# Kernel optimization log

Hardware: AMD Instinct MI355X
Metric: run time of the kernel (lower is better)

Reference implementation:

```python
import jax, jax.numpy as jnp
import numpy as np

EPS = 1e-20


def _conv(x, w, pad):
    # NCHW / OIHW conv, stride 1, symmetric padding
    return jax.lax.conv_general_dilated(
        x, w, window_strides=(1, 1),
        padding=((pad, pad), (pad, pad)),
        dimension_numbers=("NCHW", "OIHW", "NCHW"))


def _nconv(data, conf, w, b, pad):
    # normalized convolution: conv(d*c)/conv(c) + bias ; cout = conv(c)/sum(w)
    denom = _conv(conf, w, pad)
    nomin = _conv(data * conf, w, pad)
    out = nomin / (denom + EPS) + b[None, :, None, None]
    s = jnp.sum(w, axis=(1, 2, 3))  # per-out-channel kernel sum
    cout = denom / s[None, :, None, None]
    return out, cout


def _maxpool_ds(x, c):
    # 2x2/stride-2 max pool on c, gathering x at argmax positions (torch return_indices semantics)
    B, C, H, W = c.shape
    cw = c.reshape(B, C, H // 2, 2, W // 2, 2).transpose(0, 1, 2, 4, 3, 5).reshape(B, C, H // 2, W // 2, 4)
    xw = x.reshape(B, C, H // 2, 2, W // 2, 2).transpose(0, 1, 2, 4, 3, 5).reshape(B, C, H // 2, W // 2, 4)
    idx = jnp.argmax(cw, axis=-1)  # first-max tie-break, same as torch
    c_ds = jnp.take_along_axis(cw, idx[..., None], axis=-1)[..., 0] / 4.0
    x_ds = jnp.take_along_axis(xw, idx[..., None], axis=-1)[..., 0]
    return x_ds, c_ds


def _up2(x):
    return jnp.repeat(jnp.repeat(x, 2, axis=2), 2, axis=3)


def setup_inputs() -> dict:
    key = jax.random.key(0)
    ks = jax.random.split(key, 18)
    B, H, W = 8, 512, 512
    x0 = jax.random.normal(ks[0], (B, 1, H, W), dtype=jnp.float32)
    c0 = jax.random.uniform(ks[1], (B, 1, H, W), dtype=jnp.float32)

    def posw(k, shape):
        # positive kernel (the module enforces positivity via softplus hook)
        return jax.nn.softplus(jax.random.normal(k, shape, dtype=jnp.float32))

    inp = {"x0": x0, "c0": c0}
    shapes = {
        "w1": (2, 1, 5, 5), "w2": (2, 2, 5, 5), "w3": (2, 2, 5, 5),
        "w4": (2, 4, 3, 3), "w5": (2, 4, 3, 3), "w6": (2, 4, 3, 3),
        "w7": (1, 2, 1, 1),
    }
    for i, (name, shp) in enumerate(shapes.items()):
        inp[name] = posw(ks[2 + i], shp)
        inp["b" + name[1:]] = jnp.full((shp[0],), 0.01, dtype=jnp.float32)
    return inp


def reference(x0, c0, w1, b1, w2, b2, w3, b3, w4, b4, w5, b5, w6, b6, w7, b7):
    x1, c1 = _nconv(x0, c0, w1, b1, 2)
    x1, c1 = _nconv(x1, c1, w2, b2, 2)
    x1, c1 = _nconv(x1, c1, w3, b3, 2)

    x1_ds, c1_ds = _maxpool_ds(x1, c1)
    x2_ds, c2_ds = _nconv(x1_ds, c1_ds, w2, b2, 2)
    x2_ds, c2_ds = _nconv(x2_ds, c2_ds, w3, b3, 2)

    x2_dss, c2_dss = _maxpool_ds(x2_ds, c2_ds)
    x3_ds, c3_ds = _nconv(x2_dss, c2_dss, w2, b2, 2)

    x3_dss, c3_dss = _maxpool_ds(x3_ds, c3_ds)
    x4_ds, c4_ds = _nconv(x3_dss, c3_dss, w2, b2, 2)

    x4, c4 = _up2(x4_ds), _up2(c4_ds)
    x34_ds, c34_ds = _nconv(jnp.concatenate((x3_ds, x4), 1), jnp.concatenate((c3_ds, c4), 1), w4, b4, 1)

    x34, c34 = _up2(x34_ds), _up2(c34_ds)
    x23_ds, c23_ds = _nconv(jnp.concatenate((x2_ds, x34), 1), jnp.concatenate((c2_ds, c34), 1), w5, b5, 1)

    x23, c23 = _up2(x23_ds), _up2(c23_ds)
    xout, cout = _nconv(jnp.concatenate((x23, x1), 1), jnp.concatenate((c23, c1), 1), w6, b6, 1)
    xout, cout = _nconv(xout, cout, w7, b7, 0)
    return xout, cout
```

## Files before the change

### kernel.cpp

```cpp
#include <hip/hip_runtime.h>

#define EPSF 1e-20f

__device__ __forceinline__ float frcp(float x) { return __builtin_amdgcn_rcpf(x); }


struct CD8 { float2 v[8]; };
__device__ __forceinline__ CD8 load_cd8(const float2* p) {
    const float4* q = (const float4*)p;
    const float4 t0 = q[0], t1 = q[1], t2 = q[2], t3 = q[3];
    CD8 r;
    r.v[0] = make_float2(t0.x, t0.y); r.v[1] = make_float2(t0.z, t0.w);
    r.v[2] = make_float2(t1.x, t1.y); r.v[3] = make_float2(t1.z, t1.w);
    r.v[4] = make_float2(t2.x, t2.y); r.v[5] = make_float2(t2.z, t2.w);
    r.v[6] = make_float2(t3.x, t3.y); r.v[7] = make_float2(t3.z, t3.w);
    return r;
}
struct CD6 { float2 v[6]; };
__device__ __forceinline__ CD6 load_cd6(const float2* p) {
    const float4* q = (const float4*)p;
    const float4 t0 = q[0], t1 = q[1], t2 = q[2];
    CD6 r;
    r.v[0] = make_float2(t0.x, t0.y); r.v[1] = make_float2(t0.z, t0.w);
    r.v[2] = make_float2(t1.x, t1.y); r.v[3] = make_float2(t1.z, t1.w);
    r.v[4] = make_float2(t2.x, t2.y); r.v[5] = make_float2(t2.z, t2.w);
    return r;
}
__device__ __forceinline__ void fma2(float2& a, float w, float2 cd) {
    a.x = fmaf(w, cd.x, a.x);
    a.y = fmaf(w, cd.y, a.y);
}

template<int NCI, int CI0, int CINT, int K, int ROWS>
__device__ __forceinline__ void conv_core_i(const float2* __restrict__ s,
                                            const float* __restrict__ wgt,
                                            int lh, int lw,
                                            float2 acc[2][4])
{
    constexpr int JB = 2 - (K / 2);
    #pragma unroll
    for (int kh = 0; kh < K; ++kh) {
        #pragma unroll
        for (int ci = 0; ci < NCI; ++ci) {
            const CD8 cd = load_cd8(s + (ci * ROWS + lh + kh) * 72 + lw + 2);
            #pragma unroll
            for (int kw = 0; kw < K; ++kw) {
                const float w0 = wgt[((0 * CINT + CI0 + ci) * K + kh) * K + kw];
                const float w1 = wgt[((1 * CINT + CI0 + ci) * K + kh) * K + kw];
                #pragma unroll
                for (int p = 0; p < 4; ++p) {
                    const int j = p + kw + JB;
                    fma2(acc[0][p], w0, cd.v[j]);
                    fma2(acc[1][p], w1, cd.v[j]);
                }
            }
        }
    }
}

template<int LO0>
__device__ __forceinline__ void conv_low_i(const float2* __restrict__ s_lo,
                                           const float* __restrict__ wgt,
                                           int lh, int lw,
                                           float2 acc[2][4])
{
    #pragma unroll
    for (int kh = 0; kh < 3; ++kh) {
        const int rel_r = ((lh + kh - 1) >> 1) + 1;
        #pragma unroll
        for (int lci = 0; lci < 2; ++lci) {
            const CD6 cd = load_cd6(s_lo + (lci * 10 + rel_r) * 40 + (lw >> 1) + 2);
            #pragma unroll
            for (int kw = 0; kw < 3; ++kw) {
                const float w0 = wgt[((0 * 4 + LO0 + lci) * 3 + kh) * 3 + kw];
                const float w1 = wgt[((1 * 4 + LO0 + lci) * 3 + kh) * 3 + kw];
                #pragma unroll
                for (int p = 0; p < 4; ++p) {
                    const int t = p + kw - 1;
                    const int jl = ((t < 0) ? -1 : (t >> 1)) + 2;
                    fma2(acc[0][p], w0, cd.v[jl]);
                    fma2(acc[1][p], w1, cd.v[jl]);
                }
            }
        }
    }
}

template<int CINT, int K>
__device__ __forceinline__ void nconv_epilogue_i(const float* __restrict__ wgt,
                                                 const float* __restrict__ bias,
                                                 float2 acc[2][4],
                                                 float4 uo[2], float4 co4[2])
{
    #pragma unroll
    for (int c = 0; c < 2; ++c) {
        float s = 0.f;
        for (int i = 0; i < CINT * K * K; ++i) s += wgt[c * CINT * K * K + i];
        const float is = 1.0f / s;
        const float bb = bias[c];
        #pragma unroll
        for (int p = 0; p < 4; ++p) {
            const float xo = acc[c][p].y * frcp(acc[c][p].x + EPSF) + bb;
            const float cv = acc[c][p].x * is;
            (&co4[c].x)[p] = cv;
            (&uo[c].x)[p]  = xo * cv;
        }
    }
}

__global__ __launch_bounds__(256)
void enc12_fused(const float* __restrict__ x0, const float* __restrict__ c0,
                 const float* __restrict__ wA, const float* __restrict__ bA,
                 const float* __restrict__ wB, const float* __restrict__ bB,
                 float* __restrict__ uout, float* __restrict__ cout)
{
    __shared__ __align__(16) float2 in_cd[24][84];
    __shared__ __align__(16) float2 mid_cd[2][20][72];

    const int tid = threadIdx.x;
    const int bw = blockIdx.x * 64;
    const int bh = blockIdx.y * 16;
    const int b  = blockIdx.z;

    const float4* x4 = (const float4*)x0;
    const float4* c4 = (const float4*)c0;
    for (int i = tid; i < 480; i += 256) {
        const int r = i / 20, k = i % 20;
        const int gh = bh - 4 + r;
        const int gw4 = (bw >> 2) - 2 + k;
        float4 xx = make_float4(0.f, 0.f, 0.f, 0.f);
        float4 cc = make_float4(0.f, 0.f, 0.f, 0.f);
        if ((unsigned)gh < 512u && (unsigned)gw4 < 128u) {
            const int a = (b << 16) + (gh << 7) + gw4;
            xx = x4[a];
            cc = c4[a];
        }
        float4* dst = (float4*)&in_cd[r][4 * k];
        dst[0] = make_float4(cc.x, xx.x * cc.x, cc.y, xx.y * cc.y);
        dst[1] = make_float4(cc.z, xx.z * cc.z, cc.w, xx.w * cc.w);
    }

    float isA0, isA1;
    {
        float s0 = 0.f, s1 = 0.f;
        for (int i = 0; i < 25; ++i) { s0 += wA[i]; s1 += wA[25 + i]; }
        isA0 = 1.0f / s0;
        isA1 = 1.0f / s1;
    }
    __syncthreads();

    #pragma unroll
    for (int pass = 0; pass < 2; ++pass) {
        int r, g;
        bool active = true;
        if (pass == 0) { r = tid >> 4; g = tid & 15; }
        else {
            if (tid < 64) { r = 16 + (tid >> 4); g = tid & 15; }
            else if (tid < 104) { const int t = tid - 64; r = t >> 1; g = 16 + (t & 1); }
            else { active = false; r = 0; g = 0; }
        }
        if (active) {
            float2 acc[2][4];
            #pragma unroll
            for (int c = 0; c < 2; ++c)
                #pragma unroll
                for (int p = 0; p < 4; ++p) acc[c][p] = make_float2(0.f, 0.f);
            #pragma unroll
            for (int kh = 0; kh < 5; ++kh) {
                const CD8 cd = load_cd8(&in_cd[r + kh][4 * g + 2]);
                #pragma unroll
                for (int kw = 0; kw < 5; ++kw) {
                    const float w0 = wA[kh * 5 + kw];
                    const float w1 = wA[25 + kh * 5 + kw];
                    #pragma unroll
                    for (int p = 0; p < 4; ++p) {
                        fma2(acc[0][p], w0, cd.v[p + kw]);
                        fma2(acc[1][p], w1, cd.v[p + kw]);
                    }
                }
            }
            const int orow = bh + r - 2;
            const bool rok = (unsigned)orow < 512u;
            #pragma unroll
            for (int c = 0; c < 2; ++c) {
                const float is = (c == 0) ? isA0 : isA1;
                float cv[4], du[4];
                #pragma unroll
                for (int p = 0; p < 4; ++p) {
                    const int ocol = bw + 4 * g - 4 + p;
                    const bool ok = rok && (unsigned)ocol < 512u;
                    const float xo = acc[c][p].y * frcp(acc[c][p].x + EPSF) + bA[c];
                    const float v = acc[c][p].x * is;
                    cv[p] = ok ? v : 0.f;
                    du[p] = ok ? xo * v : 0.f;
                }
                float4* dst = (float4*)&mid_cd[c][r][4 * g];
                dst[0] = make_float4(cv[0], du[0], cv[1], du[1]);
                dst[1] = make_float4(cv[2], du[2], cv[3], du[3]);
            }
        }
    }
    __syncthreads();

    const int lh = tid >> 4;
    const int lw = (tid & 15) << 2;
    float2 acc[2][4];
    #pragma unroll
    for (int c = 0; c < 2; ++c)
        #pragma unroll
        for (int p = 0; p < 4; ++p) acc[c][p] = make_float2(0.f, 0.f);

    conv_core_i<2, 0, 2, 5, 20>(&mid_cd[0][0][0], wB, lh, lw, acc);

    float4 uo[2], co4[2];
    nconv_epilogue_i<2, 5>(wB, bB, acc, uo, co4);

    const int oh = bh + lh;
    #pragma unroll
    for (int c = 0; c < 2; ++c) {
        const int a = ((b * 2 + c) << 16) + (oh << 7) + ((bw + lw) >> 2);
        ((float4*)uout)[a] = uo[c];
        ((float4*)cout)[a] = co4[c];
    }
}

__global__ __launch_bounds__(256)
void enc45_fused(const float* __restrict__ inU, const float* __restrict__ inC,
                 const float* __restrict__ wA, const float* __restrict__ bA,
                 const float* __restrict__ wB, const float* __restrict__ bB,
                 float* __restrict__ uout, float* __restrict__ cout,
                 float* __restrict__ poolU, float* __restrict__ poolC)
{
    __shared__ __align__(16) float2 in_cd[2][24][84];
    __shared__ __align__(16) float2 mid_cd[2][20][72];

    const int tid = threadIdx.x;
    const int bw = blockIdx.x * 64;
    const int bh = blockIdx.y * 16;
    const int b  = blockIdx.z;

    const float4* U4 = (const float4*)inU;
    const float4* C4 = (const float4*)inC;
    for (int i = tid; i < 960; i += 256) {
        const int ci = i / 480;
        const int r = (i / 20) % 24, k = i % 20;
        const int gh = bh - 4 + r;
        const int gw4 = (bw >> 2) - 2 + k;
        float4 dd = make_float4(0.f, 0.f, 0.f, 0.f);
        float4 cc = make_float4(0.f, 0.f, 0.f, 0.f);
        if ((unsigned)gh < 256u && (unsigned)gw4 < 64u) {
            const int a = ((b * 2 + ci) << 14) + (gh << 6) + gw4;
            dd = U4[a];
            cc = C4[a];
        }
        float4* dst = (float4*)&in_cd[ci][r][4 * k];
        dst[0] = make_float4(cc.x, dd.x, cc.y, dd.y);
        dst[1] = make_float4(cc.z, dd.z, cc.w, dd.w);
    }

    float isA0, isA1;
    {
        float s0 = 0.f, s1 = 0.f;
        for (int i = 0; i < 50; ++i) { s0 += wA[i]; s1 += wA[50 + i]; }
        isA0 = 1.0f / s0;
        isA1 = 1.0f / s1;
    }
    __syncthreads();

    #pragma unroll
    for (int pass = 0; pass < 2; ++pass) {
        int r, g;
        bool active = true;
        if (pass == 0) { r = tid >> 4; g = tid & 15; }
        else {
            if (tid < 64) { r = 16 + (tid >> 4); g = tid & 15; }
            else if (tid < 104) { const int t = tid - 64; r = t >> 1; g = 16 + (t & 1); }
            else { active = false; r = 0; g = 0; }
        }
        if (active) {
            float2 acc[2][4];
            #pragma unroll
            for (int c = 0; c < 2; ++c)
                #pragma unroll
                for (int p = 0; p < 4; ++p) acc[c][p] = make_float2(0.f, 0.f);
            #pragma unroll
            for (int kh = 0; kh < 5; ++kh) {
                #pragma unroll
                for (int ci = 0; ci < 2; ++ci) {
                    const CD8 cd = load_cd8(&in_cd[ci][r + kh][4 * g + 2]);
                    #pragma unroll
                    for (int kw = 0; kw < 5; ++kw) {
                        const float w0 = wA[((0 * 2 + ci) * 5 + kh) * 5 + kw];
                        const float w1 = wA[((1 * 2 + ci) * 5 + kh) * 5 + kw];
                        #pragma unroll
                        for (int p = 0; p < 4; ++p) {
                            fma2(acc[0][p], w0, cd.v[p + kw]);
                            fma2(acc[1][p], w1, cd.v[p + kw]);
                        }
                    }
                }
            }
            const int orow = bh + r - 2;
            const bool rok = (unsigned)orow < 256u;
            #pragma unroll
            for (int c = 0; c < 2; ++c) {
                const float is = (c == 0) ? isA0 : isA1;
                float cv[4], du[4];
                #pragma unroll
                for (int p = 0; p < 4; ++p) {
                    const int ocol = bw + 4 * g - 4 + p;
                    const bool ok = rok && (unsigned)ocol < 256u;
                    const float xo = acc[c][p].y * frcp(acc[c][p].x + EPSF) + bA[c];
                    const float v = acc[c][p].x * is;
                    cv[p] = ok ? v : 0.f;
                    du[p] = ok ? xo * v : 0.f;
                }
                float4* dst = (float4*)&mid_cd[c][r][4 * g];
                dst[0] = make_float4(cv[0], du[0], cv[1], du[1]);
                dst[1] = make_float4(cv[2], du[2], cv[3], du[3]);
            }
        }
    }
    __syncthreads();

    const int lh = tid >> 4;
    const int lw = (tid & 15) << 2;
    float2 acc[2][4];
    #pragma unroll
    for (int c = 0; c < 2; ++c)
        #pragma unroll
        for (int p = 0; p < 4; ++p) acc[c][p] = make_float2(0.f, 0.f);

    conv_core_i<2, 0, 2, 5, 20>(&mid_cd[0][0][0], wB, lh, lw, acc);

    float4 uo[2], co4[2];
    nconv_epilogue_i<2, 5>(wB, bB, acc, uo, co4);

    const int oh = bh + lh;
    #pragma unroll
    for (int c = 0; c < 2; ++c) {
        const int a = ((b * 2 + c) << 14) + (oh << 6) + ((bw + lw) >> 2);
        ((float4*)uout)[a] = uo[c];
        ((float4*)cout)[a] = co4[c];
    }

    __syncthreads();
    float2* pb = &mid_cd[0][0][0];
    #pragma unroll
    for (int c = 0; c < 2; ++c) {
        float2* row = pb + (c * 16 + lh) * 64 + lw;
        #pragma unroll
        for (int p = 0; p < 4; ++p)
            row[p] = make_float2((&co4[c].x)[p], (&uo[c].x)[p]);
    }
    __syncthreads();
    #pragma unroll
    for (int rep = 0; rep < 2; ++rep) {
        const int o = tid + rep * 256;
        const int ch = o >> 8;
        const int idx = o & 255;
        const int pr = idx >> 5;
        const int pcc = idx & 31;
        const float2* base = pb + (ch * 16 + 2 * pr) * 64 + 2 * pcc;
        const float2 a0 = base[0], a1 = base[1], a2 = base[64], a3 = base[65];
        float m = a0.x, g = a0.y;
        if (a1.x > m) { m = a1.x; g = a1.y; }
        if (a2.x > m) { m = a2.x; g = a2.y; }
        if (a3.x > m) { m = a3.x; g = a3.y; }
        const int pa = ((b * 2 + ch) << 14) + (((bh >> 1) + pr) << 7) + (bw >> 1) + pcc;
        poolU[pa] = g * 0.25f;
        poolC[pa] = m * 0.25f;
    }
}

__global__ __launch_bounds__(256)
void mid_kern(const float* __restrict__ p2U, const float* __restrict__ p2C,
              const float* __restrict__ w2, const float* __restrict__ b2,
              const float* __restrict__ w4, const float* __restrict__ b4,
              float* __restrict__ x34U, float* __restrict__ x34C)
{
    __shared__ __align__(16) float2 sp_cd[2][32][88];
    __shared__ __align__(16) float2 sx3_cd[2][28][80];
    __shared__ __align__(16) float2 sp3_cd[2][14][48];
    __shared__ __align__(16) float2 sx4_cd[2][10][40];

    const int tid = threadIdx.x;
    const int bw = blockIdx.x * 64;
    const int bh = blockIdx.y * 16;
    const int b = blockIdx.z;

    const float4* U4 = (const float4*)p2U;
    const float4* C4 = (const float4*)p2C;
    for (int i = tid; i < 2 * 32 * 22; i += 256) {
        const int ci = i / 704;
        const int r  = (i / 22) % 32;
        const int cf = i % 22;
        const int gh = bh - 8 + r;
        const int gw4 = (bw >> 2) - 3 + cf;
        float4 dd = make_float4(0.f, 0.f, 0.f, 0.f);
        float4 cc = make_float4(0.f, 0.f, 0.f, 0.f);
        if ((unsigned)gh < 128u && (unsigned)gw4 < 32u) {
            const int a = ((b * 2 + ci) << 12) + (gh << 5) + gw4;
            dd = U4[a];
            cc = C4[a];
        }
        float4* dst = (float4*)&sp_cd[ci][r][cf * 4];
        dst[0] = make_float4(cc.x, dd.x, cc.y, dd.y);
        dst[1] = make_float4(cc.z, dd.z, cc.w, dd.w);
    }
    __syncthreads();

    {
        float s2[2];
        #pragma unroll
        for (int c = 0; c < 2; ++c) {
            float s = 0.f;
            for (int i = 0; i < 50; ++i) s += w2[c * 50 + i];
            s2[c] = 1.0f / s;
        }
        for (int s = tid; s < 560; s += 256) {
            const int r = s / 20;
            const int g = s % 20;
            float2 acc[2][4];
            #pragma unroll
            for (int c = 0; c < 2; ++c)
                #pragma unroll
                for (int p = 0; p < 4; ++p) acc[c][p] = make_float2(0.f, 0.f);
            #pragma unroll
            for (int kh = 0; kh < 5; ++kh) {
                #pragma unroll
                for (int ci = 0; ci < 2; ++ci) {
                    const CD8 cd = load_cd8(&sp_cd[ci][r + kh][4 * g + 2]);
                    #pragma unroll
                    for (int kw = 0; kw < 5; ++kw) {
                        const float w0 = w2[((0 * 2 + ci) * 5 + kh) * 5 + kw];
                        const float w1 = w2[((1 * 2 + ci) * 5 + kh) * 5 + kw];
                        #pragma unroll
                        for (int p = 0; p < 4; ++p) {
                            fma2(acc[0][p], w0, cd.v[p + kw]);
                            fma2(acc[1][p], w1, cd.v[p + kw]);
                        }
                    }
                }
            }
            const int orow = bh - 6 + r;
            const bool rok = (unsigned)orow < 128u;
            #pragma unroll
            for (int c = 0; c < 2; ++c) {
                float cv[4], du[4];
                #pragma unroll
                for (int p = 0; p < 4; ++p) {
                    const int ocol = bw - 8 + 4 * g + p;
                    const bool ok = rok && (unsigned)ocol < 128u;
                    const float xo = acc[c][p].y * frcp(acc[c][p].x + EPSF) + b2[c];
                    const float v = acc[c][p].x * s2[c];
                    cv[p] = ok ? v : 0.f;
                    du[p] = ok ? xo * v : 0.f;
                }
                float4* dst = (float4*)&sx3_cd[c][r][4 * g];
                dst[0] = make_float4(cv[0], du[0], cv[1], du[1]);
                dst[1] = make_float4(cv[2], du[2], cv[3], du[3]);
            }
        }
    }
    __syncthreads();

    for (int i = tid; i < 2 * 14 * 48; i += 256) {
        const int ch = i / 672;
        const int r  = (i / 48) % 14;
        const int c  = i % 48;
        const int R = (bh >> 1) - 3 + r;
        const int C = (bw >> 1) - 8 + c;
        float g = 0.f, m = 0.f;
        if (c >= 4 && c < 44 && (unsigned)R < 64u && (unsigned)C < 64u) {
            const int xr = 2 * r, xc = 2 * c - 8;
            const float2 a0 = sx3_cd[ch][xr][xc],     a1 = sx3_cd[ch][xr][xc + 1];
            const float2 a2 = sx3_cd[ch][xr + 1][xc], a3 = sx3_cd[ch][xr + 1][xc + 1];
            m = a0.x; g = a0.y;
            if (a1.x > m) { m = a1.x; g = a1.y; }
            if (a2.x > m) { m = a2.x; g = a2.y; }
            if (a3.x > m) { m = a3.x; g = a3.y; }
            g *= 0.25f; m *= 0.25f;
        }
        sp3_cd[ch][r][c] = make_float2(m, g);
    }
    __syncthreads();

    {
        float s2[2];
        #pragma unroll
        for (int c = 0; c < 2; ++c) {
            float s = 0.f;
            for (int i = 0; i < 50; ++i) s += w2[c * 50 + i];
            s2[c] = 1.0f / s;
        }
        for (int s = tid; s < 100; s += 256) {
            const int r = s / 10;
            const int g = s % 10;
            float2 acc[2][4];
            #pragma unroll
            for (int c = 0; c < 2; ++c)
                #pragma unroll
                for (int p = 0; p < 4; ++p) acc[c][p] = make_float2(0.f, 0.f);
            #pragma unroll
            for (int kh = 0; kh < 5; ++kh) {
                #pragma unroll
                for (int ci = 0; ci < 2; ++ci) {
                    const CD8 cd = load_cd8(&sp3_cd[ci][r + kh][4 * g + 2]);
                    #pragma unroll
                    for (int kw = 0; kw < 5; ++kw) {
                        const float w0 = w2[((0 * 2 + ci) * 5 + kh) * 5 + kw];
                        const float w1 = w2[((1 * 2 + ci) * 5 + kh) * 5 + kw];
                        #pragma unroll
                        for (int p = 0; p < 4; ++p) {
                            fma2(acc[0][p], w0, cd.v[p + kw]);
                            fma2(acc[1][p], w1, cd.v[p + kw]);
                        }
                    }
                }
            }
            const int orow = (bh >> 1) - 1 + r;
            const bool rok = (unsigned)orow < 64u;
            #pragma unroll
            for (int c = 0; c < 2; ++c) {
                float cv[4], du[4];
                #pragma unroll
                for (int p = 0; p < 4; ++p) {
                    const int ocol = (bw >> 1) - 4 + 4 * g + p;
                    const bool ok = rok && (unsigned)ocol < 64u;
                    const float xo = acc[c][p].y * frcp(acc[c][p].x + EPSF) + b2[c];
                    const float v = acc[c][p].x * s2[c];
                    cv[p] = ok ? v : 0.f;
                    du[p] = ok ? xo * v : 0.f;
                }
                float4* dst = (float4*)&sx4_cd[c][r][4 * g];
                dst[0] = make_float4(cv[0], du[0], cv[1], du[1]);
                dst[1] = make_float4(cv[2], du[2], cv[3], du[3]);
            }
        }
    }
    __syncthreads();

    {
        const int lh = tid >> 4;
        const int lw = (tid & 15) << 2;
        float2 acc[2][4];
        #pragma unroll
        for (int c = 0; c < 2; ++c)
            #pragma unroll
            for (int p = 0; p < 4; ++p) acc[c][p] = make_float2(0.f, 0.f);

        #pragma unroll
        for (int kh = 0; kh < 3; ++kh) {
            #pragma unroll
            for (int ci = 0; ci < 2; ++ci) {
                const CD8 cd = load_cd8(&sx3_cd[ci][lh + kh + 5][lw + 6]);
                #pragma unroll
                for (int kw = 0; kw < 3; ++kw) {
                    const float w0 = w4[((0 * 4 + ci) * 3 + kh) * 3 + kw];
                    const float w1 = w4[((1 * 4 + ci) * 3 + kh) * 3 + kw];
                    #pragma unroll
                    for (int p = 0; p < 4; ++p) {
                        const int j = p + kw + 1;
                        fma2(acc[0][p], w0, cd.v[j]);
                        fma2(acc[1][p], w1, cd.v[j]);
                    }
                }
            }
        }
        conv_low_i<2>(&sx4_cd[0][0][0], w4, lh, lw, acc);

        float4 uo[2], co4[2];
        nconv_epilogue_i<4, 3>(w4, b4, acc, uo, co4);
        #pragma unroll
        for (int c = 0; c < 2; ++c) {
            const int a = ((b * 2 + c) << 12) + ((bh + lh) << 5) + ((bw + lw) >> 2);
            ((float4*)x34U)[a] = uo[c];
            ((float4*)x34C)[a] = co4[c];
        }
    }
}

template<int CIN, int K, int LOGHW, bool IN_IS_U, bool POOL>
__global__ __launch_bounds__(256)
void nconv_tiled(const float* __restrict__ xin, const float* __restrict__ cin_,
                 const float* __restrict__ wgt, const float* __restrict__ bias,
                 float* __restrict__ uout, float* __restrict__ cout,
                 float* __restrict__ poolU, float* __restrict__ poolC)
{
    constexpr int HW = 1 << LOGHW;
    constexpr int PAD = K / 2;
    constexpr int TH = 16;
    constexpr int ROWS = TH + 2 * PAD;
    constexpr int NC4 = 18;
    __shared__ __align__(16) float2 s_cd[CIN][ROWS][72];

    const int tid = threadIdx.x;
    const int base_w = blockIdx.x * 64;
    const int base_h = blockIdx.y * TH;
    const int b = blockIdx.z;

    constexpr int SLOTS = CIN * ROWS * NC4;
    const float4* x4 = (const float4*)xin;
    const float4* c4p = (const float4*)cin_;
    for (int i = tid; i < SLOTS; i += 256) {
        const int ci = i / (ROWS * NC4);
        const int r  = (i / NC4) % ROWS;
        const int cf = i % NC4;
        const int gh = base_h - PAD + r;
        const int gw4 = (base_w >> 2) + cf - 1;
        float4 dd = make_float4(0.f, 0.f, 0.f, 0.f);
        float4 cc = make_float4(0.f, 0.f, 0.f, 0.f);
        if ((unsigned)gh < (unsigned)HW && (unsigned)gw4 < (unsigned)(HW >> 2)) {
            const int a = ((b * CIN + ci) << (2 * LOGHW - 2)) + (gh << (LOGHW - 2)) + gw4;
            const float4 xx = x4[a];
            cc = c4p[a];
            if (IN_IS_U) dd = xx;
            else dd = make_float4(xx.x * cc.x, xx.y * cc.y, xx.z * cc.z, xx.w * cc.w);
        }
        float4* dst = (float4*)&s_cd[ci][r][cf * 4];
        dst[0] = make_float4(cc.x, dd.x, cc.y, dd.y);
        dst[1] = make_float4(cc.z, dd.z, cc.w, dd.w);
    }
    __syncthreads();

    const int lh = tid >> 4;
    const int lw = (tid & 15) << 2;
    float2 acc[2][4];
    #pragma unroll
    for (int c = 0; c < 2; ++c)
        #pragma unroll
        for (int p = 0; p < 4; ++p) acc[c][p] = make_float2(0.f, 0.f);

    conv_core_i<CIN, 0, CIN, K, ROWS>(&s_cd[0][0][0], wgt, lh, lw, acc);

    float4 uo[2], co4[2];
    nconv_epilogue_i<CIN, K>(wgt, bias, acc, uo, co4);

    const int oh = base_h + lh;
    #pragma unroll
    for (int c = 0; c < 2; ++c) {
        const int a = ((b * 2 + c) << (2 * LOGHW - 2)) + (oh << (LOGHW - 2)) + ((base_w + lw) >> 2);
        ((float4*)uout)[a] = uo[c];
        ((float4*)cout)[a] = co4[c];
    }

    if (POOL) {
        __syncthreads();
        float2* pb = &s_cd[0][0][0];
        #pragma unroll
        for (int c = 0; c < 2; ++c) {
            float2* row = pb + (c * 16 + lh) * 64 + lw;
            #pragma unroll
            for (int p = 0; p < 4; ++p)
                row[p] = make_float2((&co4[c].x)[p], (&uo[c].x)[p]);
        }
        __syncthreads();
        #pragma unroll
        for (int rep = 0; rep < 2; ++rep) {
            const int o = tid + rep * 256;
            const int ch = o >> 8;
            const int idx = o & 255;
            const int pr = idx >> 5;
            const int pcc = idx & 31;
            const float2* base = pb + (ch * 16 + 2 * pr) * 64 + 2 * pcc;
            const float2 a0 = base[0], a1 = base[1], a2 = base[64], a3 = base[65];
            float m = a0.x, g = a0.y;
            if (a1.x > m) { m = a1.x; g = a1.y; }
            if (a2.x > m) { m = a2.x; g = a2.y; }
            if (a3.x > m) { m = a3.x; g = a3.y; }
            const int pa = ((b * 2 + ch) << (2 * (LOGHW - 1)))
                         + (((base_h >> 1) + pr) << (LOGHW - 1)) + (base_w >> 1) + pcc;
            poolU[pa] = g * 0.25f;
            poolC[pa] = m * 0.25f;
        }
    }
}

template<bool UP_FIRST, int LOGHW, bool FINAL>
__global__ __launch_bounds__(256)
void nconv_cat_tiled(const float* __restrict__ skU, const float* __restrict__ skC,
                     const float* __restrict__ loU, const float* __restrict__ loC,
                     const float* __restrict__ wgt, const float* __restrict__ bias,
                     float* __restrict__ uout, float* __restrict__ cout,
                     const float* __restrict__ w7, const float* __restrict__ b7)
{
    constexpr int HW = 1 << LOGHW;
    constexpr int HWL = HW >> 1;
    constexpr int TH = 16;
    constexpr int ROWS = TH + 2;
    constexpr int NC4 = 18;
    constexpr int SK0 = UP_FIRST ? 2 : 0;
    constexpr int LO0 = UP_FIRST ? 0 : 2;
    __shared__ __align__(16) float2 s_cd[2][ROWS][72];
    __shared__ __align__(16) float2 lo_cd[2][10][40];

    const int tid = threadIdx.x;
    const int base_w = blockIdx.x * 64;
    const int base_h = blockIdx.y * TH;
    const int b = blockIdx.z;

    constexpr int SLOTS = 2 * ROWS * NC4;
    const float4* sU4 = (const float4*)skU;
    const float4* sC4 = (const float4*)skC;
    for (int i = tid; i < SLOTS; i += 256) {
        const int ci = i / (ROWS * NC4);
        const int r  = (i / NC4) % ROWS;
        const int cf = i % NC4;
        const int gh = base_h - 1 + r;
        const int gw4 = (base_w >> 2) + cf - 1;
        float4 dd = make_float4(0.f, 0.f, 0.f, 0.f);
        float4 cc = make_float4(0.f, 0.f, 0.f, 0.f);
        if ((unsigned)gh < (unsigned)HW && (unsigned)gw4 < (unsigned)(HW >> 2)) {
            const int a = ((b * 2 + ci) << (2 * LOGHW - 2)) + (gh << (LOGHW - 2)) + gw4;
            dd = sU4[a];
            cc = sC4[a];
        }
        float4* dst = (float4*)&s_cd[ci][r][cf * 4];
        dst[0] = make_float4(cc.x, dd.x, cc.y, dd.y);
        dst[1] = make_float4(cc.z, dd.z, cc.w, dd.w);
    }
    constexpr int LO_SLOTS = 2 * 10 * 10;
    const int lo_r0 = (base_h >> 1) - 1;
    const int lo_c4_0 = (base_w >> 3) - 1;
    const float4* lU4 = (const float4*)loU;
    const float4* lC4 = (const float4*)loC;
    for (int i = tid; i < LO_SLOTS; i += 256) {
        const int ci = i / 100;
        const int r  = (i / 10) % 10;
        const int cf = i % 10;
        const int gr = lo_r0 + r;
        const int gc4 = lo_c4_0 + cf;
        float4 dd = make_float4(0.f, 0.f, 0.f, 0.f);
        float4 cc = make_float4(0.f, 0.f, 0.f, 0.f);
        if ((unsigned)gr < (unsigned)HWL && (unsigned)gc4 < (unsigned)(HWL >> 2)) {
            const int a = ((b * 2 + ci) << (2 * (LOGHW - 1) - 2)) + (gr << (LOGHW - 3)) + gc4;
            dd = lU4[a];
            cc = lC4[a];
        }
        float4* dst = (float4*)&lo_cd[ci][r][cf * 4];
        dst[0] = make_float4(cc.x, dd.x, cc.y, dd.y);
        dst[1] = make_float4(cc.z, dd.z, cc.w, dd.w);
    }
    __syncthreads();

    const int lh = tid >> 4;
    const int lw = (tid & 15) << 2;
    float2 acc[2][4];
    #pragma unroll
    for (int c = 0; c < 2; ++c)
        #pragma unroll
        for (int p = 0; p < 4; ++p) acc[c][p] = make_float2(0.f, 0.f);

    conv_core_i<2, SK0, 4, 3, ROWS>(&s_cd[0][0][0], wgt, lh, lw, acc);
    conv_low_i<LO0>(&lo_cd[0][0][0], wgt, lh, lw, acc);

    float4 uo[2], co4[2];
    nconv_epilogue_i<4, 3>(wgt, bias, acc, uo, co4);

    const int oh = base_h + lh;
    if (FINAL) {
        const float w70 = w7[0], w71 = w7[1], bb7 = b7[0];
        const float inv = frcp(w70 + w71);
        float4 xo4, cc4;
        #pragma unroll
        for (int p = 0; p < 4; ++p) {
            const float d1 = w70 * (&co4[0].x)[p] + w71 * (&co4[1].x)[p];
            (&xo4.x)[p] = (w70 * (&uo[0].x)[p] + w71 * (&uo[1].x)[p]) * frcp(d1 + EPSF) + bb7;
            (&cc4.x)[p] = d1 * inv;
        }
        const int a = (b << (2 * LOGHW - 2)) + (oh << (LOGHW - 2)) + ((base_w + lw) >> 2);
        ((float4*)uout)[a] = xo4;
        ((float4*)uout)[(1 << 19) + a] = cc4;
    } else {
        #pragma unroll
        for (int c = 0; c < 2; ++c) {
            const int a = ((b * 2 + c) << (2 * LOGHW - 2)) + (oh << (LOGHW - 2)) + ((base_w + lw) >> 2);
            ((float4*)uout)[a] = uo[c];
            ((float4*)cout)[a] = co4[c];
        }
    }
}

extern "C" void kernel_launch(void* const* d_in, const int* in_sizes, int n_in,
                              void* d_out, int out_size, void* d_ws, size_t ws_size,
                              hipStream_t stream) {
    (void)in_sizes; (void)n_in; (void)out_size; (void)ws_size;
    const float* x0 = (const float*)d_in[0];
    const float* c0 = (const float*)d_in[1];
    const float* w1 = (const float*)d_in[2];  const float* b1 = (const float*)d_in[3];
    const float* w2 = (const float*)d_in[4];  const float* b2 = (const float*)d_in[5];
    const float* w3 = (const float*)d_in[6];  const float* b3 = (const float*)d_in[7];
    const float* w4 = (const float*)d_in[8];  const float* b4 = (const float*)d_in[9];
    const float* w5 = (const float*)d_in[10]; const float* b5 = (const float*)d_in[11];
    const float* w6 = (const float*)d_in[12]; const float* b6 = (const float*)d_in[13];
    const float* w7 = (const float*)d_in[14]; const float* b7 = (const float*)d_in[15];

    float* ws = (float*)d_ws;
    const size_t S512 = 8ull * 2 * 512 * 512;
    const size_t S256 = 8ull * 2 * 256 * 256;
    const size_t S128 = 8ull * 2 * 128 * 128;

    float* X1x = ws;            float* X1c = ws + S512;
    float* Ax  = ws + 2 * S512; float* Ac  = ws + 3 * S512;
    float* Bx  = ws + 4 * S512; float* Bc  = ws + 5 * S512;
    float* x23x = Ax;               float* x23c = Ax + S256;
    float* x2x  = Ax + 2 * S256;    float* x2c  = Ax + 3 * S256;
    float* p1x  = Ax + 4 * S256;    float* p1c  = Ax + 5 * S256;
    float* p2x  = Bx + 2 * S128;    float* p2c  = Bx + 3 * S128;
    float* x34x = Bx + 4 * S128;    float* x34c = Bx + 5 * S128;

    enc12_fused<<<dim3(8, 32, 8), 256, 0, stream>>>(
        x0, c0, w1, b1, w2, b2, Bx, Bc);
    nconv_tiled<2, 5, 9, true, true><<<dim3(8, 32, 8), 256, 0, stream>>>(
        Bx, Bc, w3, b3, X1x, X1c, p1x, p1c);
    enc45_fused<<<dim3(4, 16, 8), 256, 0, stream>>>(
        p1x, p1c, w2, b2, w3, b3, x2x, x2c, p2x, p2c);
    mid_kern<<<dim3(2, 8, 8), 256, 0, stream>>>(
        p2x, p2c, w2, b2, w4, b4, x34x, x34c);
    nconv_cat_tiled<false, 8, false><<<dim3(4, 16, 8), 256, 0, stream>>>(
        x2x, x2c, x34x, x34c, w5, b5, x23x, x23c, nullptr, nullptr);
    nconv_cat_tiled<true, 9, true><<<dim3(8, 32, 8), 256, 0, stream>>>(
        X1x, X1c, x23x, x23c, w6, b6, (float*)d_out, nullptr, w7, b7);
}
```

Before: 125.7 us.

## Fuse first three encoder nconv layers and maxpool into one kernel

Extends the fused encoder kernel from two to three 5x5 normalized convolutions, with a larger input halo, and adds the 2x2 argmax pooling at the end. This removes the full-resolution intermediate write and read of the second-layer output and drops one kernel launch. In exchange, each block recomputes a wider halo for layers one and two and uses more shared memory, which may lower occupancy.

Result: slower. 130.1 us (+3.5%).

```diff
diff --git a/kernel.cpp b/kernel.cpp
--- a/kernel.cpp
+++ b/kernel.cpp
@@ -109,13 +109,17 @@
 }
 
 __global__ __launch_bounds__(256)
-void enc12_fused(const float* __restrict__ x0, const float* __restrict__ c0,
-                 const float* __restrict__ wA, const float* __restrict__ bA,
-                 const float* __restrict__ wB, const float* __restrict__ bB,
-                 float* __restrict__ uout, float* __restrict__ cout)
+void enc123_fused(const float* __restrict__ x0, const float* __restrict__ c0,
+                  const float* __restrict__ w1, const float* __restrict__ b1,
+                  const float* __restrict__ w2, const float* __restrict__ b2,
+                  const float* __restrict__ w3, const float* __restrict__ b3,
+                  float* __restrict__ X1u, float* __restrict__ X1c,
+                  float* __restrict__ p1u, float* __restrict__ p1c)
 {
-    __shared__ __align__(16) float2 in_cd[24][84];
-    __shared__ __align__(16) float2 mid_cd[2][20][72];
+    __shared__ __align__(16) float2 smem[6528];
+    float2* m1  = smem;
+    float2* inb = smem + 3648;
+    float2* m2  = smem + 3648;
 
     const int tid = threadIdx.x;
     const int bw = blockIdx.x * 64;
@@ -124,9 +128,9 @@
 
     const float4* x4 = (const float4*)x0;
     const float4* c4 = (const float4*)c0;
-    for (int i = tid; i < 480; i += 256) {
+    for (int i = tid; i < 560; i += 256) {
         const int r = i / 20, k = i % 20;
-        const int gh = bh - 4 + r;
+        const int gh = bh - 6 + r;
         const int gw4 = (bw >> 2) - 2 + k;
         float4 xx = make_float4(0.f, 0.f, 0.f, 0.f);
         float4 cc = make_float4(0.f, 0.f, 0.f, 0.f);
@@ -135,24 +139,76 @@
             xx = x4[a];
             cc = c4[a];
         }
-        float4* dst = (float4*)&in_cd[r][4 * k];
+        float4* dst = (float4*)(inb + r * 80 + 4 * k);
         dst[0] = make_float4(cc.x, xx.x * cc.x, cc.y, xx.y * cc.y);
         dst[1] = make_float4(cc.z, xx.z * cc.z, cc.w, xx.w * cc.w);
     }
 
-    float isA0, isA1;
+    float is1[2], is2[2];
     {
         float s0 = 0.f, s1 = 0.f;
-        for (int i = 0; i < 25; ++i) { s0 += wA[i]; s1 += wA[25 + i]; }
-        isA0 = 1.0f / s0;
-        isA1 = 1.0f / s1;
+        for (int i = 0; i < 25; ++i) { s0 += w1[i]; s1 += w1[25 + i]; }
+        is1[0] = 1.0f / s0; is1[1] = 1.0f / s1;
+        float t0 = 0.f, t1 = 0.f;
+        for (int i = 0; i < 50; ++i) { t0 += w2[i]; t1 += w2[50 + i]; }
+        is2[0] = 1.0f / t0; is2[1] = 1.0f / t1;
     }
     __syncthreads();
 
     #pragma unroll
     for (int pass = 0; pass < 2; ++pass) {
-        int r, g;
-        bool active = true;
+        int r, g; bool active = true;
+        if (pass == 0) { r = tid >> 4; g = tid & 15; }
+        else {
+            if (tid < 128) { r = 16 + (tid >> 4); g = tid & 15; }
+            else if (tid < 200) { const int t = tid - 128; r = t / 3; g = 16 + t % 3; }
+            else { active = false; r = 0; g = 0; }
+        }
+        if (active) {
+            float2 acc[2][4];
+            #pragma unroll
+            for (int c = 0; c < 2; ++c)
+                #pragma unroll
+                for (int p = 0; p < 4; ++p) acc[c][p] = make_float2(0.f, 0.f);
+            #pragma unroll
+            for (int kh = 0; kh < 5; ++kh) {
+                const CD8 cd = load_cd8(inb + (r + kh) * 80 + 4 * g);
+                #pragma unroll
+                for (int kw = 0; kw < 5; ++kw) {
+                    const float wa = w1[kh * 5 + kw];
+                    const float wb = w1[25 + kh * 5 + kw];
+                    #pragma unroll
+                    for (int p = 0; p < 4; ++p) {
+                        fma2(acc[0][p], wa, cd.v[p + kw]);
+                        fma2(acc[1][p], wb, cd.v[p + kw]);
+                    }
+                }
+            }
+            const int orow = bh - 4 + r;
+            const bool rok = (unsigned)orow < 512u;
+            #pragma unroll
+            for (int c = 0; c < 2; ++c) {
+                float cv[4], du[4];
+                #pragma unroll
+                for (int p = 0; p < 4; ++p) {
+                    const int ocol = bw - 6 + 4 * g + p;
+                    const bool ok = rok && (unsigned)ocol < 512u;
+                    const float xo = acc[c][p].y * frcp(acc[c][p].x + EPSF) + b1[c];
+                    const float v = acc[c][p].x * is1[c];
+                    cv[p] = ok ? v : 0.f;
+                    du[p] = ok ? xo * v : 0.f;
+                }
+                float4* dst = (float4*)(m1 + (c * 24 + r) * 76 + 4 * g);
+                dst[0] = make_float4(cv[0], du[0], cv[1], du[1]);
+                dst[1] = make_float4(cv[2], du[2], cv[3], du[3]);
+            }
+        }
+    }
+    __syncthreads();
+
+    #pragma unroll
+    for (int pass = 0; pass < 2; ++pass) {
+        int r, g; bool active = true;
         if (pass == 0) { r = tid >> 4; g = tid & 15; }
         else {
             if (tid < 64) { r = 16 + (tid >> 4); g = tid & 15; }
@@ -167,34 +223,36 @@
                 for (int p = 0; p < 4; ++p) acc[c][p] = make_float2(0.f, 0.f);
             #pragma unroll
             for (int kh = 0; kh < 5; ++kh) {
-                const CD8 cd = load_cd8(&in_cd[r + kh][4 * g + 2]);
-                #pragma unroll
-                for (int kw = 0; kw < 5; ++kw) {
-                    const float w0 = wA[kh * 5 + kw];
-                    const float w1 = wA[25 + kh * 5 + kw];
+                #pragma unroll
+                for (int ci = 0; ci < 2; ++ci) {
+                    const CD8 cd = load_cd8(m1 + (ci * 24 + r + kh) * 76 + 4 * g);
                     #pragma unroll
-                    for (int p = 0; p < 4; ++p) {
-                        fma2(acc[0][p], w0, cd.v[p + kw]);
-                        fma2(acc[1][p], w1, cd.v[p + kw]);
+                    for (int kw = 0; kw < 5; ++kw) {
+                        const float wa = w2[((0 * 2 + ci) * 5 + kh) * 5 + kw];
+                        const float wb = w2[((1 * 2 + ci) * 5 + kh) * 5 + kw];
+                        #pragma unroll
+                        for (int p = 0; p < 4; ++p) {
+                            fma2(acc[0][p], wa, cd.v[p + kw]);
+                            fma2(acc[1][p], wb, cd.v[p + kw]);
+                        }
                     }
                 }
             }
-            const int orow = bh + r - 2;
+            const int orow = bh - 2 + r;
             const bool rok = (unsigned)orow < 512u;
             #pragma unroll
             for (int c = 0; c < 2; ++c) {
-                const float is = (c == 0) ? isA0 : isA1;
                 float cv[4], du[4];
                 #pragma unroll
                 for (int p = 0; p < 4; ++p) {
-                    const int ocol = bw + 4 * g - 4 + p;
+                    const int ocol = bw - 4 + 4 * g + p;
                     const bool ok = rok && (unsigned)ocol < 512u;
-                    const float xo = acc[c][p].y * frcp(acc[c][p].x + EPSF) + bA[c];
-                    const float v = acc[c][p].x * is;
+                    const float xo = acc[c][p].y * frcp(acc[c][p].x + EPSF) + b2[c];
+                    const float v = acc[c][p].x * is2[c];
                     cv[p] = ok ? v : 0.f;
                     du[p] = ok ? xo * v : 0.f;
                 }
-                float4* dst = (float4*)&mid_cd[c][r][4 * g];
+                float4* dst = (float4*)(m2 + (c * 20 + r) * 72 + 4 * g);
                 dst[0] = make_float4(cv[0], du[0], cv[1], du[1]);
                 dst[1] = make_float4(cv[2], du[2], cv[3], du[3]);
             }
@@ -210,17 +268,45 @@
         #pragma unroll
         for (int p = 0; p < 4; ++p) acc[c][p] = make_float2(0.f, 0.f);
 
-    conv_core_i<2, 0, 2, 5, 20>(&mid_cd[0][0][0], wB, lh, lw, acc);
+    conv_core_i<2, 0, 2, 5, 20>(m2, w3, lh, lw, acc);
 
     float4 uo[2], co4[2];
-    nconv_epilogue_i<2, 5>(wB, bB, acc, uo, co4);
+    nconv_epilogue_i<2, 5>(w3, b3, acc, uo, co4);
 
     const int oh = bh + lh;
     #pragma unroll
     for (int c = 0; c < 2; ++c) {
         const int a = ((b * 2 + c) << 16) + (oh << 7) + ((bw + lw) >> 2);
-        ((float4*)uout)[a] = uo[c];
-        ((float4*)cout)[a] = co4[c];
+        ((float4*)X1u)[a] = uo[c];
+        ((float4*)X1c)[a] = co4[c];
+    }
+
+    __syncthreads();
+    float2* pb = m1;
+    #pragma unroll
+    for (int c = 0; c < 2; ++c) {
+        float2* row = pb + (c * 16 + lh) * 64 + lw;
+        #pragma unroll
+        for (int p = 0; p < 4; ++p)
+            row[p] = make_float2((&co4[c].x)[p], (&uo[c].x)[p]);
+    }
+    __syncthreads();
+    #pragma unroll
+    for (int rep = 0; rep < 2; ++rep) {
+        const int o = tid + rep * 256;
+        const int ch = o >> 8;
+        const int idx = o & 255;
+        const int pr = idx >> 5;
+        const int pcc = idx & 31;
+        const float2* base = pb + (ch * 16 + 2 * pr) * 64 + 2 * pcc;
+        const float2 a0 = base[0], a1 = base[1], a2 = base[64], a3 = base[65];
+        float m = a0.x, g = a0.y;
+        if (a1.x > m) { m = a1.x; g = a1.y; }
+        if (a2.x > m) { m = a2.x; g = a2.y; }
+        if (a3.x > m) { m = a3.x; g = a3.y; }
+        const int pa = ((b * 2 + ch) << 16) + (((bh >> 1) + pr) << 8) + (bw >> 1) + pcc;
+        p1u[pa] = g * 0.25f;
+        p1c[pa] = m * 0.25f;
     }
 }
 
@@ -577,102 +663,6 @@
             const int a = ((b * 2 + c) << 12) + ((bh + lh) << 5) + ((bw + lw) >> 2);
             ((float4*)x34U)[a] = uo[c];
             ((float4*)x34C)[a] = co4[c];
-        }
-    }
-}
-
-template<int CIN, int K, int LOGHW, bool IN_IS_U, bool POOL>
-__global__ __launch_bounds__(256)
-void nconv_tiled(const float* __restrict__ xin, const float* __restrict__ cin_,
-                 const float* __restrict__ wgt, const float* __restrict__ bias,
-                 float* __restrict__ uout, float* __restrict__ cout,
-                 float* __restrict__ poolU, float* __restrict__ poolC)
-{
-    constexpr int HW = 1 << LOGHW;
-    constexpr int PAD = K / 2;
-    constexpr int TH = 16;
-    constexpr int ROWS = TH + 2 * PAD;
-    constexpr int NC4 = 18;
-    __shared__ __align__(16) float2 s_cd[CIN][ROWS][72];
-
-    const int tid = threadIdx.x;
-    const int base_w = blockIdx.x * 64;
-    const int base_h = blockIdx.y * TH;
-    const int b = blockIdx.z;
-
-    constexpr int SLOTS = CIN * ROWS * NC4;
-    const float4* x4 = (const float4*)xin;
-    const float4* c4p = (const float4*)cin_;
-    for (int i = tid; i < SLOTS; i += 256) {
-        const int ci = i / (ROWS * NC4);
-        const int r  = (i / NC4) % ROWS;
-        const int cf = i % NC4;
-        const int gh = base_h - PAD + r;
-        const int gw4 = (base_w >> 2) + cf - 1;
-        float4 dd = make_float4(0.f, 0.f, 0.f, 0.f);
-        float4 cc = make_float4(0.f, 0.f, 0.f, 0.f);
-        if ((unsigned)gh < (unsigned)HW && (unsigned)gw4 < (unsigned)(HW >> 2)) {
-            const int a = ((b * CIN + ci) << (2 * LOGHW - 2)) + (gh << (LOGHW - 2)) + gw4;
-            const float4 xx = x4[a];
-            cc = c4p[a];
-            if (IN_IS_U) dd = xx;
-            else dd = make_float4(xx.x * cc.x, xx.y * cc.y, xx.z * cc.z, xx.w * cc.w);
-        }
-        float4* dst = (float4*)&s_cd[ci][r][cf * 4];
-        dst[0] = make_float4(cc.x, dd.x, cc.y, dd.y);
-        dst[1] = make_float4(cc.z, dd.z, cc.w, dd.w);
-    }
-    __syncthreads();
-
-    const int lh = tid >> 4;
-    const int lw = (tid & 15) << 2;
-    float2 acc[2][4];
-    #pragma unroll
-    for (int c = 0; c < 2; ++c)
-        #pragma unroll
-        for (int p = 0; p < 4; ++p) acc[c][p] = make_float2(0.f, 0.f);
-
-    conv_core_i<CIN, 0, CIN, K, ROWS>(&s_cd[0][0][0], wgt, lh, lw, acc);
-
-    float4 uo[2], co4[2];
-    nconv_epilogue_i<CIN, K>(wgt, bias, acc, uo, co4);
-
-    const int oh = base_h + lh;
-    #pragma unroll
-    for (int c = 0; c < 2; ++c) {
-        const int a = ((b * 2 + c) << (2 * LOGHW - 2)) + (oh << (LOGHW - 2)) + ((base_w + lw) >> 2);
-        ((float4*)uout)[a] = uo[c];
-        ((float4*)cout)[a] = co4[c];
-    }
-
-    if (POOL) {
-        __syncthreads();
-        float2* pb = &s_cd[0][0][0];
-        #pragma unroll
-        for (int c = 0; c < 2; ++c) {
-            float2* row = pb + (c * 16 + lh) * 64 + lw;
-            #pragma unroll
-            for (int p = 0; p < 4; ++p)
-                row[p] = make_float2((&co4[c].x)[p], (&uo[c].x)[p]);
-        }
-        __syncthreads();
-        #pragma unroll
-        for (int rep = 0; rep < 2; ++rep) {
-            const int o = tid + rep * 256;
-            const int ch = o >> 8;
-            const int idx = o & 255;
-            const int pr = idx >> 5;
-            const int pcc = idx & 31;
-            const float2* base = pb + (ch * 16 + 2 * pr) * 64 + 2 * pcc;
-            const float2 a0 = base[0], a1 = base[1], a2 = base[64], a3 = base[65];
-            float m = a0.x, g = a0.y;
-            if (a1.x > m) { m = a1.x; g = a1.y; }
-            if (a2.x > m) { m = a2.x; g = a2.y; }
-            if (a3.x > m) { m = a3.x; g = a3.y; }
-            const int pa = ((b * 2 + ch) << (2 * (LOGHW - 1)))
-                         + (((base_h >> 1) + pr) << (LOGHW - 1)) + (base_w >> 1) + pcc;
-            poolU[pa] = g * 0.25f;
-            poolC[pa] = m * 0.25f;
         }
     }
 }
@@ -802,18 +792,16 @@
     const size_t S128 = 8ull * 2 * 128 * 128;
 
     float* X1x = ws;            float* X1c = ws + S512;
-    float* Ax  = ws + 2 * S512; float* Ac  = ws + 3 * S512;
-    float* Bx  = ws + 4 * S512; float* Bc  = ws + 5 * S512;
+    float* Ax  = ws + 2 * S512;
+    float* Bx  = ws + 4 * S512;
     float* x23x = Ax;               float* x23c = Ax + S256;
     float* x2x  = Ax + 2 * S256;    float* x2c  = Ax + 3 * S256;
     float* p1x  = Ax + 4 * S256;    float* p1c  = Ax + 5 * S256;
     float* p2x  = Bx + 2 * S128;    float* p2c  = Bx + 3 * S128;
     float* x34x = Bx + 4 * S128;    float* x34c = Bx + 5 * S128;
 
-    enc12_fused<<<dim3(8, 32, 8), 256, 0, stream>>>(
-        x0, c0, w1, b1, w2, b2, Bx, Bc);
-    nconv_tiled<2, 5, 9, true, true><<<dim3(8, 32, 8), 256, 0, stream>>>(
-        Bx, Bc, w3, b3, X1x, X1c, p1x, p1c);
+    enc123_fused<<<dim3(8, 32, 8), 256, 0, stream>>>(
+        x0, c0, w1, b1, w2, b2, w3, b3, X1x, X1c, p1x, p1c);
     enc45_fused<<<dim3(4, 16, 8), 256, 0, stream>>>(
         p1x, p1c, w2, b2, w3, b3, x2x, x2c, p2x, p2c);
     mid_kern<<<dim3(2, 8, 8), 256, 0, stream>>>(
```
